# Performance work log

Hardware: AMD Instinct MI355X
Metric: run time of the kernel (lower is better)

## Reference

```python
import jax, jax.numpy as jnp
import numpy as np

B, S, H, D = 8, 2048, 16, 64  # batch, seq, heads, head_dim
DM = H * D                    # d_model = 1024
W = 4                         # compression window / stride


def setup_inputs() -> dict:
    key = jax.random.key(0)
    ks = jax.random.split(key, 6)
    return {
        "pre_q": jax.random.normal(ks[0], (B, S, H, D), dtype=jnp.float32),
        "pre_k": jax.random.normal(ks[1], (B, S, H, D), dtype=jnp.float32),
        "pre_v": jax.random.normal(ks[2], (B, S, H, D), dtype=jnp.float32),
        "k_conv_kernel": jax.random.normal(ks[3], (W, D, D), dtype=jnp.float32) * (1.0 / np.sqrt(W * D)),
        "k_conv_bias": jnp.zeros((D,), dtype=jnp.float32),
        "v_conv_kernel": jax.random.normal(ks[4], (W, D, D), dtype=jnp.float32) * (1.0 / np.sqrt(W * D)),
        "v_conv_bias": jnp.zeros((D,), dtype=jnp.float32),
        "output_weights": jax.random.normal(ks[5], (DM, DM), dtype=jnp.float32) * (1.0 / np.sqrt(DM)),
        "compression_window": W,
    }


def _compress(x, kernel, bias, window):
    # x: [B, H, S, D] -> strided valid conv along seq -> [B, H, Sc, D]
    b, h, s, d = x.shape
    x2 = x.reshape(b * h, s, d)  # NWC
    y = jax.lax.conv_general_dilated(
        x2, kernel, window_strides=(window,), padding="VALID",
        dimension_numbers=("NWC", "WIO", "NWC")) + bias
    return y.reshape(b, h, -1, d)


def reference(pre_q, pre_k, pre_v, k_conv_kernel, k_conv_bias,
              v_conv_kernel, v_conv_bias, output_weights, compression_window):
    b, s, h, d = pre_q.shape
    q = jnp.transpose(pre_q, (0, 2, 1, 3))  # [B,H,S,D]
    k = jnp.transpose(pre_k, (0, 2, 1, 3))
    v = jnp.transpose(pre_v, (0, 2, 1, 3))
    kc = _compress(k, k_conv_kernel, k_conv_bias, compression_window)  # [B,H,Sc,D]
    vc = _compress(v, v_conv_kernel, v_conv_bias, compression_window)
    scale = 1.0 / np.sqrt(d).astype(np.float32)
    scores = jnp.einsum("bhsd,bhtd->bhst", q, kc) * scale  # [B,H,S,Sc]
    attn = jax.nn.softmax(scores, axis=-1)
    out = jnp.einsum("bhst,bhtd->bhsd", attn, vc)  # [B,H,S,D]
    out = jnp.transpose(out, (0, 2, 1, 3)).reshape(b, s, h * d)  # [B,S,DM]
    return out @ output_weights  # [B,S,DM]
```

## Files before the change

### kernel.cpp

```cpp
#include <hip/hip_runtime.h>
#include <hip/hip_bf16.h>
#include <math.h>

#define B_   8
#define S_   2048
#define H_   16
#define D_   64
#define DM_  1024
#define W_   4
#define SC_  512

typedef float f32x4 __attribute__((ext_vector_type(4)));
typedef short bf16x8 __attribute__((ext_vector_type(8)));
typedef short bf16x4 __attribute__((ext_vector_type(4)));

static __device__ inline short f2bf(float f) {
    union { float f; unsigned u; } v; v.f = f;
    unsigned r = v.u + 0x7fffu + ((v.u >> 16) & 1u);
    return (short)(r >> 16);
}

static __device__ inline short bfc(float f) {
    __hip_bfloat16 h = __float2bfloat16(f);
    union { __hip_bfloat16 h; short s; } u; u.h = h; return u.s;
}

static __device__ inline float fexp2(float x) {
    float r; asm("v_exp_f32 %0, %1" : "=v"(r) : "v"(x)); return r;
}

static __device__ inline void gll16(const void* g, void* l) {
    __builtin_amdgcn_global_load_lds(
        (const __attribute__((address_space(1))) unsigned int*)g,
        (__attribute__((address_space(3))) unsigned int*)l, 16, 0, 0);
}

__global__ __launch_bounds__(256) void wtrans_kernel(
    const float* __restrict__ Wg, short* __restrict__ Wt)
{
    __shared__ float ws[64][68];
    const int tid = threadIdx.x;
    const int n0 = blockIdx.x * 64, k0 = blockIdx.y * 64;
    #pragma unroll
    for (int i = 0; i < 4; ++i) {
        int idx = i * 256 + tid;
        int row = idx >> 4, c4 = idx & 15;
        float4 v = *(const float4*)(Wg + (size_t)(k0 + row) * 1024 + n0 + c4 * 4);
        *(float4*)(&ws[row][c4 * 4]) = v;
    }
    __syncthreads();
    #pragma unroll
    for (int i = 0; i < 2; ++i) {
        int idx = i * 256 + tid;
        int n = idx >> 3, kc8 = idx & 7;
        bf16x8 o;
        #pragma unroll
        for (int j = 0; j < 8; ++j) o[j] = f2bf(ws[kc8 * 8 + j][n]);
        *(bf16x8*)(Wt + (size_t)(n0 + n) * 1024 + k0 + kc8 * 8) = o;
    }
}

__global__ __launch_bounds__(256) void prep_kernel(
    const float* __restrict__ kk, const float* __restrict__ vk,
    short* __restrict__ BkT)
{
    __shared__ float ws[64][68];
    const int tid = threadIdx.x;
    const int k0 = blockIdx.x * 64;
    const float* src = blockIdx.y ? vk : kk;
    short* dst = BkT + (size_t)blockIdx.y * 64 * 256;
    #pragma unroll
    for (int i = 0; i < 4; ++i) {
        int idx = i * 256 + tid;
        int row = idx >> 4, c4 = idx & 15;
        float4 v = *(const float4*)(src + (size_t)(k0 + row) * 64 + c4 * 4);
        *(float4*)(&ws[row][c4 * 4]) = v;
    }
    __syncthreads();
    #pragma unroll
    for (int i = 0; i < 2; ++i) {
        int idx = i * 256 + tid;
        int n = idx >> 3, kc8 = idx & 7;
        bf16x8 o;
        #pragma unroll
        for (int j = 0; j < 8; ++j) o[j] = f2bf(ws[kc8 * 8 + j][n]);
        *(bf16x8*)(dst + (size_t)n * 256 + k0 + kc8 * 8) = o;
    }
}

template<int TR>
__global__ __launch_bounds__(256) void compress_mfma(
    const float* __restrict__ x,
    const short* __restrict__ bkt,
    const float* __restrict__ bias,
    short* __restrict__ y)
{
    __shared__ __align__(16) char Ah[16384];
    __shared__ __align__(16) char Al[16384];
    __shared__ __align__(16) char Bs[32768];
    const int tid  = threadIdx.x;
    const int bid  = (blockIdx.x & 7) * 256 + (blockIdx.x >> 3);
    const int tile = bid & 15;
    const int bh   = bid >> 4;
    const int h    = bh & 15;
    const int b    = bh >> 4;
    const int t0   = tile * 32;
    const int s0   = t0 * 4;

    #pragma unroll
    for (int i = 0; i < 8; ++i) {
        int idx = i * 256 + tid;
        int sl = idx >> 4, c4 = idx & 15;
        float4 v = *(const float4*)(x + (((size_t)(b * S_ + s0 + sl) * H_ + h) * D_) + c4 * 4);
        int tl = sl >> 2, k = (sl & 3) * 64 + c4 * 4;
        bf16x4 h4, l4;
        #pragma unroll
        for (int j = 0; j < 4; ++j) {
            float f = ((const float*)&v)[j];
            short hs = f2bf(f);
            union { unsigned u; float f; } hf; hf.u = ((unsigned)(unsigned short)hs) << 16;
            h4[j] = hs;
            l4[j] = f2bf(f - hf.f);
        }
        int base = (tl * 256 + k) * 2;
        int sw = (tl & 7) << 4;
        *(bf16x4*)(Ah + (base ^ sw)) = h4;
        *(bf16x4*)(Al + (base ^ sw)) = l4;
    }
    #pragma unroll
    for (int i = 0; i < 8; ++i) {
        int idx = i * 256 + tid;
        int dr = idx >> 5, part = idx & 31;
        bf16x8 bv = *(const bf16x8*)(bkt + dr * 256 + part * 8);
        *(bf16x8*)(Bs + ((dr * 512 + part * 16) ^ ((dr & 7) << 4))) = bv;
    }

    const int w = tid >> 6, ln = tid & 63, ln15 = ln & 15, hi = ln >> 4;
    const int wm = w & 1, wn = w >> 1;
    f32x4 acc[2];
    #pragma unroll
    for (int nf = 0; nf < 2; ++nf) {
        float bv = bias[wn * 32 + nf * 16 + ln15];
        acc[nf] = (f32x4){bv, bv, bv, bv};
    }
    __syncthreads();

    const int arow = wm * 16 + ln15;
    const int asw  = (arow & 7) << 4;
    #pragma unroll
    for (int kst = 0; kst < 16; ++kst) {
        const char* Asel = (kst < 8) ? Ah : Al;
        int kb = (kst & 7) * 64 + hi * 16;
        bf16x8 af = *(const bf16x8*)(Asel + ((arow * 512 + kb) ^ asw));
        #pragma unroll
        for (int nf = 0; nf < 2; ++nf) {
            int br = wn * 32 + nf * 16 + ln15;
            bf16x8 b8 = *(const bf16x8*)(Bs + ((br * 512 + kb) ^ ((br & 7) << 4)));
            acc[nf] = __builtin_amdgcn_mfma_f32_16x16x32_bf16(af, b8, acc[nf], 0, 0, 0);
        }
    }

    #pragma unroll
    for (int nf = 0; nf < 2; ++nf) {
        int dout = wn * 32 + nf * 16 + ln15;
        #pragma unroll
        for (int r = 0; r < 4; ++r) {
            float vv = acc[nf][r];
            if (!TR) {
                int t = t0 + wm * 16 + hi * 4 + r;
                y[((size_t)bh * SC_ + t) * 64 + dout] = f2bf(vv);
            } else {
                int p = r + 4 * wm + 8 * hi;
                y[((size_t)bh * 64 + dout) * SC_ + t0 + p] = f2bf(vv);
            }
        }
    }
}

__global__ __launch_bounds__(1024) void attn_kernel(
    const float* __restrict__ q,
    const short* __restrict__ kc,
    const short* __restrict__ vct,
    short* __restrict__ xb)
{
    extern __shared__ __align__(16) char smem[];
    char* klds = smem;
    char* vlds = smem + 65536;

    const int tid  = threadIdx.x;
    const int bid  = (blockIdx.x & 7) * 64 + (blockIdx.x >> 3);
    const int qc   = bid & 3;
    const int bh   = bid >> 2;
    const int h    = bh & 15;
    const int b    = bh >> 4;
    const int w    = tid >> 6;
    const int ln   = tid & 63;
    const int ln15 = ln & 15;
    const int hi   = ln >> 4;
    const int sbase = qc * 512 + w * 32;
    const int swz  = (ln15 & 7) << 4;

    const short* kg = kc + (size_t)bh * SC_ * 64;
    const short* vg = vct + (size_t)bh * 64 * SC_;

    #pragma unroll
    for (int i = 0; i < 4; ++i) {
        int idx = i * 1024 + tid;
        int row = idx >> 3, part = idx & 7;
        bf16x8 kv = *(const bf16x8*)(kg + idx * 8);
        *(bf16x8*)(klds + ((row * 128 + part * 16) ^ ((row & 7) << 4))) = kv;
    }
    #pragma unroll
    for (int i = 0; i < 4; ++i) {
        int idx = i * 1024 + tid;
        int row = idx >> 6, part = idx & 63;
        bf16x8 vv = *(const bf16x8*)(vg + idx * 8);
        *(bf16x8*)(vlds + ((row * 1024 + part * 16) ^ ((row & 7) << 4))) = vv;
    }

    bf16x8 qb[2][2];
    {
        const float qs = 0.18033688011112042f;
        #pragma unroll
        for (int qf = 0; qf < 2; ++qf) {
            const float* qrow = q + (((size_t)(b * S_ + sbase + qf * 16 + ln15)) * H_ + h) * D_;
            #pragma unroll
            for (int dblk = 0; dblk < 2; ++dblk) {
                const float* p = qrow + dblk * 32 + hi * 8;
                #pragma unroll
                for (int j = 0; j < 8; ++j) qb[qf][dblk][j] = bfc(p[j] * qs);
            }
        }
    }

    const char* kp0 = klds + ln15 * 128 + ((hi * 16) ^ swz);
    const char* kp1 = klds + ln15 * 128 + ((64 + hi * 16) ^ swz);
    const char* vp0 = vlds + ln15 * 1024 + ((hi * 16) ^ swz);
    const char* vp1 = vlds + ln15 * 1024 + ((64 + hi * 16) ^ swz);

    f32x4 oa0[4], oa1[4];
    #pragma unroll
    for (int ns = 0; ns < 4; ++ns) {
        oa0[ns] = (f32x4){0.f, 0.f, 0.f, 0.f};
        oa1[ns] = (f32x4){0.f, 0.f, 0.f, 0.f};
    }
    float mrun0 = -1e30f, lrun0 = 0.f;
    float mrun1 = -1e30f, lrun1 = 0.f;

    __syncthreads();

    #pragma unroll
    for (int kt = 0; kt < 8; ++kt) {
        f32x4 d0[4], d1[4];
        __builtin_amdgcn_s_setprio(1);
        #pragma unroll
        for (int ks = 0; ks < 4; ++ks) {
            bf16x8 ka0 = *(const bf16x8*)(kp0 + kt * 8192 + ks * 2048);
            bf16x8 ka1 = *(const bf16x8*)(kp1 + kt * 8192 + ks * 2048);
            d0[ks] = __builtin_amdgcn_mfma_f32_16x16x32_bf16(ka0, qb[0][0], (f32x4){0.f,0.f,0.f,0.f}, 0, 0, 0);
            d0[ks] = __builtin_amdgcn_mfma_f32_16x16x32_bf16(ka1, qb[0][1], d0[ks], 0, 0, 0);
            d1[ks] = __builtin_amdgcn_mfma_f32_16x16x32_bf16(ka0, qb[1][0], (f32x4){0.f,0.f,0.f,0.f}, 0, 0, 0);
            d1[ks] = __builtin_amdgcn_mfma_f32_16x16x32_bf16(ka1, qb[1][1], d1[ks], 0, 0, 0);
        }
        __builtin_amdgcn_s_setprio(0);

        float tm0 = -1e30f, tm1 = -1e30f;
        #pragma unroll
        for (int ks = 0; ks < 4; ++ks)
            #pragma unroll
            for (int r = 0; r < 4; ++r) {
                tm0 = fmaxf(tm0, d0[ks][r]);
                tm1 = fmaxf(tm1, d1[ks][r]);
            }
        tm0 = fmaxf(tm0, __shfl_xor(tm0, 16));
        tm0 = fmaxf(tm0, __shfl_xor(tm0, 32));
        tm1 = fmaxf(tm1, __shfl_xor(tm1, 16));
        tm1 = fmaxf(tm1, __shfl_xor(tm1, 32));

        if (!__all(tm0 <= mrun0 + 11.0f)) {
            float mn = fmaxf(mrun0, tm0);
            float f = fexp2(mrun0 - mn);
            mrun0 = mn;
            lrun0 *= f;
            float fr[4];
            #pragma unroll
            for (int r = 0; r < 4; ++r) fr[r] = __shfl(f, hi * 4 + r);
            #pragma unroll
            for (int ns = 0; ns < 4; ++ns)
                #pragma unroll
                for (int r = 0; r < 4; ++r) oa0[ns][r] *= fr[r];
        }
        if (!__all(tm1 <= mrun1 + 11.0f)) {
            float mn = fmaxf(mrun1, tm1);
            float f = fexp2(mrun1 - mn);
            mrun1 = mn;
            lrun1 *= f;
            float fr[4];
            #pragma unroll
            for (int r = 0; r < 4; ++r) fr[r] = __shfl(f, hi * 4 + r);
            #pragma unroll
            for (int ns = 0; ns < 4; ++ns)
                #pragma unroll
                for (int r = 0; r < 4; ++r) oa1[ns][r] *= fr[r];
        }

        bf16x8 pa0[2], pa1[2];
        float lp0 = 0.f, lp1 = 0.f;
        #pragma unroll
        for (int ks = 0; ks < 4; ++ks)
            #pragma unroll
            for (int r = 0; r < 4; ++r) {
                float e0 = fexp2(d0[ks][r] - mrun0);
                float e1 = fexp2(d1[ks][r] - mrun1);
                lp0 += e0; lp1 += e1;
                pa0[ks >> 1][(ks & 1) * 4 + r] = bfc(e0);
                pa1[ks >> 1][(ks & 1) * 4 + r] = bfc(e1);
            }
        lp0 += __shfl_xor(lp0, 16);
        lp0 += __shfl_xor(lp0, 32);
        lp1 += __shfl_xor(lp1, 16);
        lp1 += __shfl_xor(lp1, 32);
        lrun0 += lp0;
        lrun1 += lp1;

        __builtin_amdgcn_s_setprio(1);
        #pragma unroll
        for (int ns = 0; ns < 4; ++ns) {
            bf16x8 vb0 = *(const bf16x8*)(vp0 + ns * 16384 + kt * 128);
            bf16x8 vb1 = *(const bf16x8*)(vp1 + ns * 16384 + kt * 128);
            oa0[ns] = __builtin_amdgcn_mfma_f32_16x16x32_bf16(pa0[0], vb0, oa0[ns], 0, 0, 0);
            oa0[ns] = __builtin_amdgcn_mfma_f32_16x16x32_bf16(pa0[1], vb1, oa0[ns], 0, 0, 0);
            oa1[ns] = __builtin_amdgcn_mfma_f32_16x16x32_bf16(pa1[0], vb0, oa1[ns], 0, 0, 0);
            oa1[ns] = __builtin_amdgcn_mfma_f32_16x16x32_bf16(pa1[1], vb1, oa1[ns], 0, 0, 0);
        }
        __builtin_amdgcn_s_setprio(0);
    }

    float li0[4], li1[4];
    #pragma unroll
    for (int r = 0; r < 4; ++r) {
        li0[r] = 1.f / __shfl(lrun0, hi * 4 + r);
        li1[r] = 1.f / __shfl(lrun1, hi * 4 + r);
    }
    #pragma unroll
    for (int ns = 0; ns < 4; ++ns)
        #pragma unroll
        for (int r = 0; r < 4; ++r) {
            size_t i0 = ((size_t)(b * S_ + sbase + hi * 4 + r)) * DM_ + h * 64 + ns * 16 + ln15;
            xb[i0] = f2bf(oa0[ns][r] * li0[r]);
            size_t i1 = ((size_t)(b * S_ + sbase + 16 + hi * 4 + r)) * DM_ + h * 64 + ns * 16 + ln15;
            xb[i1] = f2bf(oa1[ns][r] * li1[r]);
        }
}

__global__ __launch_bounds__(256) void proj_kernel(
    const short* __restrict__ Xb,
    const short* __restrict__ Wt,
    float* __restrict__ out)
{
    __shared__ __align__(16) short As[128 * 64];
    __shared__ __align__(16) short Bs[128 * 64];
    const int tid  = threadIdx.x;
    const int wid  = tid >> 6;
    const int ln   = tid & 63;
    const int ln15 = ln & 15;
    const int hi   = ln >> 4;
    const int wr   = wid >> 1, wc = wid & 1;
    const int bid  = (blockIdx.x & 7) * 128 + (blockIdx.x >> 3);
    const int tn   = bid & 7, tm = bid >> 3;
    const int m0   = tm * 128, n0 = tn * 128;
    const int spart = tid & 7;

    f32x4 acc[4][4];
    #pragma unroll
    for (int i = 0; i < 4; ++i)
        #pragma unroll
        for (int j = 0; j < 4; ++j) acc[i][j] = (f32x4){0.f, 0.f, 0.f, 0.f};

    for (int k0 = 0; k0 < 1024; k0 += 64) {
        #pragma unroll
        for (int i = 0; i < 4; ++i) {
            int row = (i * 256 + tid) >> 3;
            int ldsoff = __builtin_amdgcn_readfirstlane((i * 256 + (tid & ~63)) * 16);
            gll16(Xb + (size_t)(m0 + row) * 1024 + k0 + spart * 8, (char*)As + ldsoff);
            gll16(Wt + (size_t)(n0 + row) * 1024 + k0 + spart * 8, (char*)Bs + ldsoff);
        }
        __syncthreads();

        #pragma unroll
        for (int ks = 0; ks < 2; ++ks) {
            bf16x8 af[4], bfr[4];
            #pragma unroll
            for (int mf = 0; mf < 4; ++mf)
                af[mf] = *(const bf16x8*)((const char*)As + (wr * 64 + mf * 16 + ln15) * 128 + ks * 64 + hi * 16);
            #pragma unroll
            for (int nf = 0; nf < 4; ++nf)
                bfr[nf] = *(const bf16x8*)((const char*)Bs + (wc * 64 + nf * 16 + ln15) * 128 + ks * 64 + hi * 16);
            #pragma unroll
            for (int mf = 0; mf < 4; ++mf)
                #pragma unroll
                for (int nf = 0; nf < 4; ++nf)
                    acc[mf][nf] = __builtin_amdgcn_mfma_f32_16x16x32_bf16(af[mf], bfr[nf], acc[mf][nf], 0, 0, 0);
        }
        __syncthreads();
    }

    #pragma unroll
    for (int mf = 0; mf < 4; ++mf)
        #pragma unroll
        for (int nf = 0; nf < 4; ++nf)
            #pragma unroll
            for (int r = 0; r < 4; ++r)
                out[(size_t)(m0 + wr * 64 + mf * 16 + hi * 4 + r) * 1024 + n0 + wc * 64 + nf * 16 + ln15] =
                    acc[mf][nf][r];
}

extern "C" void kernel_launch(void* const* d_in, const int* in_sizes, int n_in,
                              void* d_out, int out_size, void* d_ws, size_t ws_size,
                              hipStream_t stream) {
    const float* pre_q = (const float*)d_in[0];
    const float* pre_k = (const float*)d_in[1];
    const float* pre_v = (const float*)d_in[2];
    const float* kkern = (const float*)d_in[3];
    const float* kbias = (const float*)d_in[4];
    const float* vkern = (const float*)d_in[5];
    const float* vbias = (const float*)d_in[6];
    const float* wout  = (const float*)d_in[7];
    float* out = (float*)d_out;

    short* Xb  = (short*)d_ws;
    short* kcb = Xb + (size_t)(B_ * S_) * DM_;
    short* vct = kcb + (size_t)B_ * H_ * SC_ * D_;
    short* Wtb = vct + (size_t)B_ * H_ * SC_ * D_;
    short* BkT = Wtb + (size_t)DM_ * DM_;

    prep_kernel<<<dim3(4, 2), 256, 0, stream>>>(kkern, vkern, BkT);
    wtrans_kernel<<<dim3(16, 16), 256, 0, stream>>>(wout, Wtb);
    compress_mfma<0><<<B_ * H_ * 16, 256, 0, stream>>>(pre_k, BkT, kbias, kcb);
    compress_mfma<1><<<B_ * H_ * 16, 256, 0, stream>>>(pre_v, BkT + 64 * 256, vbias, vct);
    attn_kernel<<<B_ * H_ * (S_ / 512), 1024, 131072, stream>>>(pre_q, kcb, vct, Xb);
    proj_kernel<<<DM_ / 128 * ((B_ * S_) / 128), 256, 0, stream>>>(Xb, Wtb, out);
}
```

Measured before the change: 169.9 us.

## Stage K/V in two halves to halve attention LDS and raise occupancy

The attention kernel now loads the compressed K and V tiles into shared memory in two phases of 256 keys each instead of all 512 at once. This cuts LDS per block from 128 KB to 64 KB, so two 1024-thread blocks can share a CU, and launch bounds now request a higher minimum occupancy. The cost is an extra barrier between phases with no prefetch overlap. The tighter launch bound may also force register spills.

```diff
diff --git a/kernel.cpp b/kernel.cpp
--- a/kernel.cpp
+++ b/kernel.cpp
@@ -177,15 +177,14 @@
     }
 }
 
-__global__ __launch_bounds__(1024) void attn_kernel(
+__global__ __launch_bounds__(1024, 8) void attn_kernel(
     const float* __restrict__ q,
     const short* __restrict__ kc,
     const short* __restrict__ vct,
     short* __restrict__ xb)
 {
-    extern __shared__ __align__(16) char smem[];
-    char* klds = smem;
-    char* vlds = smem + 65536;
+    __shared__ __align__(16) char klds[32768];
+    __shared__ __align__(16) char vlds[32768];
 
     const int tid  = threadIdx.x;
     const int bid  = (blockIdx.x & 7) * 64 + (blockIdx.x >> 3);
@@ -203,20 +202,8 @@
     const short* kg = kc + (size_t)bh * SC_ * 64;
     const short* vg = vct + (size_t)bh * 64 * SC_;
 
-    #pragma unroll
-    for (int i = 0; i < 4; ++i) {
-        int idx = i * 1024 + tid;
-        int row = idx >> 3, part = idx & 7;
-        bf16x8 kv = *(const bf16x8*)(kg + idx * 8);
-        *(bf16x8*)(klds + ((row * 128 + part * 16) ^ ((row & 7) << 4))) = kv;
-    }
-    #pragma unroll
-    for (int i = 0; i < 4; ++i) {
-        int idx = i * 1024 + tid;
-        int row = idx >> 6, part = idx & 63;
-        bf16x8 vv = *(const bf16x8*)(vg + idx * 8);
-        *(bf16x8*)(vlds + ((row * 1024 + part * 16) ^ ((row & 7) << 4))) = vv;
-    }
+    const int krow = tid >> 3, kpart = tid & 7;
+    const int vrow = tid >> 5, vpart = tid & 31;
 
     bf16x8 qb[2][2];
     {
@@ -235,8 +222,8 @@
 
     const char* kp0 = klds + ln15 * 128 + ((hi * 16) ^ swz);
     const char* kp1 = klds + ln15 * 128 + ((64 + hi * 16) ^ swz);
-    const char* vp0 = vlds + ln15 * 1024 + ((hi * 16) ^ swz);
-    const char* vp1 = vlds + ln15 * 1024 + ((64 + hi * 16) ^ swz);
+    const char* vp0 = vlds + ln15 * 512 + ((hi * 16) ^ swz);
+    const char* vp1 = vlds + ln15 * 512 + ((64 + hi * 16) ^ swz);
 
     f32x4 oa0[4], oa1[4];
     #pragma unroll
@@ -247,93 +234,111 @@
     float mrun0 = -1e30f, lrun0 = 0.f;
     float mrun1 = -1e30f, lrun1 = 0.f;
 
-    __syncthreads();
-
-    #pragma unroll
-    for (int kt = 0; kt < 8; ++kt) {
-        f32x4 d0[4], d1[4];
-        __builtin_amdgcn_s_setprio(1);
-        #pragma unroll
-        for (int ks = 0; ks < 4; ++ks) {
-            bf16x8 ka0 = *(const bf16x8*)(kp0 + kt * 8192 + ks * 2048);
-            bf16x8 ka1 = *(const bf16x8*)(kp1 + kt * 8192 + ks * 2048);
-            d0[ks] = __builtin_amdgcn_mfma_f32_16x16x32_bf16(ka0, qb[0][0], (f32x4){0.f,0.f,0.f,0.f}, 0, 0, 0);
-            d0[ks] = __builtin_amdgcn_mfma_f32_16x16x32_bf16(ka1, qb[0][1], d0[ks], 0, 0, 0);
-            d1[ks] = __builtin_amdgcn_mfma_f32_16x16x32_bf16(ka0, qb[1][0], (f32x4){0.f,0.f,0.f,0.f}, 0, 0, 0);
-            d1[ks] = __builtin_amdgcn_mfma_f32_16x16x32_bf16(ka1, qb[1][1], d1[ks], 0, 0, 0);
-        }
-        __builtin_amdgcn_s_setprio(0);
-
-        float tm0 = -1e30f, tm1 = -1e30f;
-        #pragma unroll
-        for (int ks = 0; ks < 4; ++ks)
-            #pragma unroll
-            for (int r = 0; r < 4; ++r) {
-                tm0 = fmaxf(tm0, d0[ks][r]);
-                tm1 = fmaxf(tm1, d1[ks][r]);
-            }
-        tm0 = fmaxf(tm0, __shfl_xor(tm0, 16));
-        tm0 = fmaxf(tm0, __shfl_xor(tm0, 32));
-        tm1 = fmaxf(tm1, __shfl_xor(tm1, 16));
-        tm1 = fmaxf(tm1, __shfl_xor(tm1, 32));
-
-        if (!__all(tm0 <= mrun0 + 11.0f)) {
-            float mn = fmaxf(mrun0, tm0);
-            float f = fexp2(mrun0 - mn);
-            mrun0 = mn;
-            lrun0 *= f;
-            float fr[4];
-            #pragma unroll
-            for (int r = 0; r < 4; ++r) fr[r] = __shfl(f, hi * 4 + r);
-            #pragma unroll
-            for (int ns = 0; ns < 4; ++ns)
-                #pragma unroll
-                for (int r = 0; r < 4; ++r) oa0[ns][r] *= fr[r];
-        }
-        if (!__all(tm1 <= mrun1 + 11.0f)) {
-            float mn = fmaxf(mrun1, tm1);
-            float f = fexp2(mrun1 - mn);
-            mrun1 = mn;
-            lrun1 *= f;
-            float fr[4];
-            #pragma unroll
-            for (int r = 0; r < 4; ++r) fr[r] = __shfl(f, hi * 4 + r);
-            #pragma unroll
-            for (int ns = 0; ns < 4; ++ns)
-                #pragma unroll
-                for (int r = 0; r < 4; ++r) oa1[ns][r] *= fr[r];
-        }
-
-        bf16x8 pa0[2], pa1[2];
-        float lp0 = 0.f, lp1 = 0.f;
-        #pragma unroll
-        for (int ks = 0; ks < 4; ++ks)
-            #pragma unroll
-            for (int r = 0; r < 4; ++r) {
-                float e0 = fexp2(d0[ks][r] - mrun0);
-                float e1 = fexp2(d1[ks][r] - mrun1);
-                lp0 += e0; lp1 += e1;
-                pa0[ks >> 1][(ks & 1) * 4 + r] = bfc(e0);
-                pa1[ks >> 1][(ks & 1) * 4 + r] = bfc(e1);
-            }
-        lp0 += __shfl_xor(lp0, 16);
-        lp0 += __shfl_xor(lp0, 32);
-        lp1 += __shfl_xor(lp1, 16);
-        lp1 += __shfl_xor(lp1, 32);
-        lrun0 += lp0;
-        lrun1 += lp1;
-
-        __builtin_amdgcn_s_setprio(1);
-        #pragma unroll
-        for (int ns = 0; ns < 4; ++ns) {
-            bf16x8 vb0 = *(const bf16x8*)(vp0 + ns * 16384 + kt * 128);
-            bf16x8 vb1 = *(const bf16x8*)(vp1 + ns * 16384 + kt * 128);
-            oa0[ns] = __builtin_amdgcn_mfma_f32_16x16x32_bf16(pa0[0], vb0, oa0[ns], 0, 0, 0);
-            oa0[ns] = __builtin_amdgcn_mfma_f32_16x16x32_bf16(pa0[1], vb1, oa0[ns], 0, 0, 0);
-            oa1[ns] = __builtin_amdgcn_mfma_f32_16x16x32_bf16(pa1[0], vb0, oa1[ns], 0, 0, 0);
-            oa1[ns] = __builtin_amdgcn_mfma_f32_16x16x32_bf16(pa1[1], vb1, oa1[ns], 0, 0, 0);
-        }
-        __builtin_amdgcn_s_setprio(0);
+    #pragma unroll
+    for (int ph = 0; ph < 2; ++ph) {
+        if (ph) __syncthreads();
+        #pragma unroll
+        for (int i = 0; i < 2; ++i) {
+            int row = krow + i * 128;
+            bf16x8 kv = *(const bf16x8*)(kg + (ph * 256 + row) * 64 + kpart * 8);
+            *(bf16x8*)(klds + ((row * 128 + kpart * 16) ^ ((row & 7) << 4))) = kv;
+        }
+        #pragma unroll
+        for (int i = 0; i < 2; ++i) {
+            int row = vrow + i * 32;
+            bf16x8 vv = *(const bf16x8*)(vg + (size_t)row * SC_ + ph * 256 + vpart * 8);
+            *(bf16x8*)(vlds + ((row * 512 + vpart * 16) ^ ((row & 7) << 4))) = vv;
+        }
+        __syncthreads();
+
+        #pragma unroll
+        for (int kt = 0; kt < 4; ++kt) {
+            f32x4 d0[4], d1[4];
+            __builtin_amdgcn_s_setprio(1);
+            #pragma unroll
+            for (int ks = 0; ks < 4; ++ks) {
+                bf16x8 ka0 = *(const bf16x8*)(kp0 + kt * 8192 + ks * 2048);
+                bf16x8 ka1 = *(const bf16x8*)(kp1 + kt * 8192 + ks * 2048);
+                d0[ks] = __builtin_amdgcn_mfma_f32_16x16x32_bf16(ka0, qb[0][0], (f32x4){0.f,0.f,0.f,0.f}, 0, 0, 0);
+                d0[ks] = __builtin_amdgcn_mfma_f32_16x16x32_bf16(ka1, qb[0][1], d0[ks], 0, 0, 0);
+                d1[ks] = __builtin_amdgcn_mfma_f32_16x16x32_bf16(ka0, qb[1][0], (f32x4){0.f,0.f,0.f,0.f}, 0, 0, 0);
+                d1[ks] = __builtin_amdgcn_mfma_f32_16x16x32_bf16(ka1, qb[1][1], d1[ks], 0, 0, 0);
+            }
+            __builtin_amdgcn_s_setprio(0);
+
+            float m0a = fmaxf(fmaxf(d0[0][0], d0[0][1]), fmaxf(d0[0][2], d0[0][3]));
+            float m0b = fmaxf(fmaxf(d0[1][0], d0[1][1]), fmaxf(d0[1][2], d0[1][3]));
+            float m0c = fmaxf(fmaxf(d0[2][0], d0[2][1]), fmaxf(d0[2][2], d0[2][3]));
+            float m0d = fmaxf(fmaxf(d0[3][0], d0[3][1]), fmaxf(d0[3][2], d0[3][3]));
+            float tm0 = fmaxf(fmaxf(m0a, m0b), fmaxf(m0c, m0d));
+            float m1a = fmaxf(fmaxf(d1[0][0], d1[0][1]), fmaxf(d1[0][2], d1[0][3]));
+            float m1b = fmaxf(fmaxf(d1[1][0], d1[1][1]), fmaxf(d1[1][2], d1[1][3]));
+            float m1c = fmaxf(fmaxf(d1[2][0], d1[2][1]), fmaxf(d1[2][2], d1[2][3]));
+            float m1d = fmaxf(fmaxf(d1[3][0], d1[3][1]), fmaxf(d1[3][2], d1[3][3]));
+            float tm1 = fmaxf(fmaxf(m1a, m1b), fmaxf(m1c, m1d));
+            tm0 = fmaxf(tm0, __shfl_xor(tm0, 16));
+            tm0 = fmaxf(tm0, __shfl_xor(tm0, 32));
+            tm1 = fmaxf(tm1, __shfl_xor(tm1, 16));
+            tm1 = fmaxf(tm1, __shfl_xor(tm1, 32));
+
+            if (!__all(tm0 <= mrun0 + 11.0f)) {
+                float mn = fmaxf(mrun0, tm0);
+                float f = fexp2(mrun0 - mn);
+                mrun0 = mn;
+                lrun0 *= f;
+                float fr[4];
+                #pragma unroll
+                for (int r = 0; r < 4; ++r) fr[r] = __shfl(f, hi * 4 + r);
+                #pragma unroll
+                for (int ns = 0; ns < 4; ++ns)
+                    #pragma unroll
+                    for (int r = 0; r < 4; ++r) oa0[ns][r] *= fr[r];
+            }
+            if (!__all(tm1 <= mrun1 + 11.0f)) {
+                float mn = fmaxf(mrun1, tm1);
+                float f = fexp2(mrun1 - mn);
+                mrun1 = mn;
+                lrun1 *= f;
+                float fr[4];
+                #pragma unroll
+                for (int r = 0; r < 4; ++r) fr[r] = __shfl(f, hi * 4 + r);
+                #pragma unroll
+                for (int ns = 0; ns < 4; ++ns)
+                    #pragma unroll
+                    for (int r = 0; r < 4; ++r) oa1[ns][r] *= fr[r];
+            }
+
+            bf16x8 pa0[2], pa1[2];
+            float lp0 = 0.f, lp1 = 0.f;
+            #pragma unroll
+            for (int ks = 0; ks < 4; ++ks)
+                #pragma unroll
+                for (int r = 0; r < 4; ++r) {
+                    float e0 = fexp2(d0[ks][r] - mrun0);
+                    float e1 = fexp2(d1[ks][r] - mrun1);
+                    lp0 += e0; lp1 += e1;
+                    pa0[ks >> 1][(ks & 1) * 4 + r] = bfc(e0);
+                    pa1[ks >> 1][(ks & 1) * 4 + r] = bfc(e1);
+                }
+            lp0 += __shfl_xor(lp0, 16);
+            lp0 += __shfl_xor(lp0, 32);
+            lp1 += __shfl_xor(lp1, 16);
+            lp1 += __shfl_xor(lp1, 32);
+            lrun0 += lp0;
+            lrun1 += lp1;
+
+            __builtin_amdgcn_s_setprio(1);
+            #pragma unroll
+            for (int ns = 0; ns < 4; ++ns) {
+                bf16x8 vb0 = *(const bf16x8*)(vp0 + ns * 8192 + kt * 128);
+                bf16x8 vb1 = *(const bf16x8*)(vp1 + ns * 8192 + kt * 128);
+                oa0[ns] = __builtin_amdgcn_mfma_f32_16x16x32_bf16(pa0[0], vb0, oa0[ns], 0, 0, 0);
+                oa0[ns] = __builtin_amdgcn_mfma_f32_16x16x32_bf16(pa0[1], vb1, oa0[ns], 0, 0, 0);
+                oa1[ns] = __builtin_amdgcn_mfma_f32_16x16x32_bf16(pa1[0], vb0, oa1[ns], 0, 0, 0);
+                oa1[ns] = __builtin_amdgcn_mfma_f32_16x16x32_bf16(pa1[1], vb1, oa1[ns], 0, 0, 0);
+            }
+            __builtin_amdgcn_s_setprio(0);
+        }
     }
 
     float li0[4], li1[4];
@@ -438,6 +443,6 @@
     wtrans_kernel<<<dim3(16, 16), 256, 0, stream>>>(wout, Wtb);
     compress_mfma<0><<<B_ * H_ * 16, 256, 0, stream>>>(pre_k, BkT, kbias, kcb);
     compress_mfma<1><<<B_ * H_ * 16, 256, 0, stream>>>(pre_v, BkT + 64 * 256, vbias, vct);
-    attn_kernel<<<B_ * H_ * (S_ / 512), 1024, 131072, stream>>>(pre_q, kcb, vct, Xb);
+    attn_kernel<<<B_ * H_ * (S_ / 512), 1024, 0, stream>>>(pre_q, kcb, vct, Xb);
     proj_kernel<<<DM_ / 128 * ((B_ * S_) / 128), 256, 0, stream>>>(Xb, Wtb, out);
 }
```

Measured after the change: 422.7 us. 2.49x slower.
